# Kernel tuning notes

Hardware: AMD Instinct MI355X
Metric: run time of the kernel (lower is better)

## Reference

```python
import jax, jax.numpy as jnp
import numpy as np

DECAY = 0.25
THRESHOLD = 1.0
TIME_STEPS = 20

@jax.custom_vjp
def spike(v):
    return (v > 0).astype(v.dtype)

def _spike_fwd(v):
    return (v > 0).astype(v.dtype), v

def _spike_bwd(v, g):
    return (g / (1.0 + jnp.abs(v)) ** 2,)

spike.defvjp(_spike_fwd, _spike_bwd)


def setup_inputs() -> dict:
    key = jax.random.key(0)
    k_x, k_w1, k_b1, k_w2, k_b2 = jax.random.split(key, 5)
    B = 32768
    x = jax.random.normal(k_x, (B, 784), dtype=jnp.float32)
    # nn.Linear-style init scales
    W1 = jax.random.normal(k_w1, (128, 784), dtype=jnp.float32) / np.sqrt(784)
    b1 = jax.random.normal(k_b1, (128,), dtype=jnp.float32) / np.sqrt(784)
    W2 = jax.random.normal(k_w2, (10, 128), dtype=jnp.float32) / np.sqrt(128)
    b2 = jax.random.normal(k_b2, (10,), dtype=jnp.float32) / np.sqrt(128)
    return {"x": x, "W1": W1, "b1": b1, "W2": W2, "b2": b2}


def reference(x, W1, b1, W2, b2):
    B = x.shape[0]
    # Input current is constant across timesteps; compute the first GEMM once.
    cur1 = x @ W1.T + b1  # [B, 128]

    def step(carry, _):
        mem1, mem2 = carry
        mem1 = mem1 * DECAY + cur1
        spk1 = spike(mem1 - THRESHOLD)
        mem1 = mem1 * (1.0 - spk1)
        mem2 = mem2 * DECAY + spk1 @ W2.T + b2
        spk2 = spike(mem2 - THRESHOLD)
        mem2 = mem2 * (1.0 - spk2)
        return (mem1, mem2), (spk1, spk2)

    init = (jnp.zeros((B, 128), x.dtype), jnp.zeros((B, 10), x.dtype))
    _, (spk1_rec, spk2_rec) = jax.lax.scan(step, init, None, length=TIME_STEPS)
    output = spk2_rec.sum(axis=0)  # [B, 10]
    return output, spk1_rec  # spk1_rec: [T, B, 128]
```

## Files before the change

### kernel.cpp

```cpp
#include <hip/hip_runtime.h>
#include <cstddef>


constexpr int BROWS  = 64;
constexpr int BK     = 16;
constexpr int NJ     = 128;
constexpr int KDIM   = 784;
constexpr int NO     = 10;
constexpr int TSTEPS = 20;

__global__ __launch_bounds__(256, 2) void snn_fused(
    const float* __restrict__ x,
    const float* __restrict__ W1,
    const float* __restrict__ b1,
    const float* __restrict__ W2,
    const float* __restrict__ b2,
    float* __restrict__ out,
    int B)
{
    __shared__ alignas(16) float xs[BK][68];
    __shared__ alignas(16) float ws[BK][192];
    __shared__ alignas(16) float4 w2s[NJ][3];
    __shared__ unsigned smaskW[2][BROWS][17];
    __shared__ float b2s[12];

    const int t  = threadIdx.x;
    const int tx = t & 15;
    const int ty = t >> 4;
    const int r0 = blockIdx.x * BROWS;

    for (int e = t; e < NJ * 3; e += 256) {
        int og = e % 3, j = e / 3;
        float sc = __int_as_float((127 - (j & 31)) << 23);
        float vv[4];
        #pragma unroll
        for (int c = 0; c < 4; ++c) {
            int o = og * 4 + c;
            vv[c] = (o < NO) ? W2[o * NJ + j] * sc : 0.0f;
        }
        float4 v; v.x = vv[0]; v.y = vv[1]; v.z = vv[2]; v.w = vv[3];
        w2s[j][og] = v;
    }
    if (t < 12) b2s[t] = (t < NO) ? b2[t] : 0.0f;

    float acc[4][8], cur[4][8];
    #pragma unroll
    for (int rr = 0; rr < 4; ++rr)
        #pragma unroll
        for (int jj = 0; jj < 8; ++jj) { acc[rr][jj] = 0.0f; cur[rr][jj] = 0.0f; }

    const int xrow = t >> 2, xkf = (t & 3) * 4;
    const int wj   = t >> 1, wkf = (t & 1) * 8;
    const int wco  = wj >> 3, wci = wj & 7;
    const float* xrp = x  + (size_t)(r0 + xrow) * KDIM + xkf;
    const float* wrp = W1 + (size_t)wj * KDIM + wkf;

    #pragma unroll 1
    for (int tt = 0; tt < 49; ++tt) {
        const int k0 = tt * BK;
        float4 xv = *(const float4*)(xrp + k0);
        float4 wa = *(const float4*)(wrp + k0);
        float4 wb = *(const float4*)(wrp + k0 + 4);
        xs[xkf + 0][xrow] = xv.x; xs[xkf + 1][xrow] = xv.y;
        xs[xkf + 2][xrow] = xv.z; xs[xkf + 3][xrow] = xv.w;
        float* wp0 = &ws[wkf][wco * 12 + wci];
        wp0[0]    = wa.x; wp0[192]  = wa.y; wp0[384]  = wa.z; wp0[576]  = wa.w;
        wp0[768]  = wb.x; wp0[960]  = wb.y; wp0[1152] = wb.z; wp0[1344] = wb.w;
        __syncthreads();
        #pragma unroll
        for (int kk = 0; kk < BK; ++kk) {
            float4 xr  = *(const float4*)&xs[kk][ty * 4];
            float4 wva = *(const float4*)&ws[kk][tx * 12];
            float4 wvb = *(const float4*)&ws[kk][tx * 12 + 4];
            float xf[4] = {xr.x, xr.y, xr.z, xr.w};
            float wf[8] = {wva.x, wva.y, wva.z, wva.w, wvb.x, wvb.y, wvb.z, wvb.w};
            #pragma unroll
            for (int rr = 0; rr < 4; ++rr)
                #pragma unroll
                for (int jj = 0; jj < 8; ++jj)
                    acc[rr][jj] = fmaf(xf[rr], wf[jj], acc[rr][jj]);
        }
        __syncthreads();
        if (tt == 19) {
            #pragma unroll
            for (int rr = 0; rr < 4; ++rr)
                #pragma unroll
                for (int jj = 0; jj < 8; ++jj) { cur[rr][jj] = acc[rr][jj]; acc[rr][jj] = 0.0f; }
        } else if (tt == 39) {
            #pragma unroll
            for (int rr = 0; rr < 4; ++rr)
                #pragma unroll
                for (int jj = 0; jj < 8; ++jj) { cur[rr][jj] = cur[rr][jj] + acc[rr][jj]; acc[rr][jj] = 0.0f; }
        }
    }
    {
        const float* b1p = b1 + tx * 8;
        float4 ba = *(const float4*)b1p, bb = *(const float4*)(b1p + 4);
        float bf[8] = {ba.x, ba.y, ba.z, ba.w, bb.x, bb.y, bb.z, bb.w};
        #pragma unroll
        for (int rr = 0; rr < 4; ++rr)
            #pragma unroll
            for (int jj = 0; jj < 8; ++jj)
                cur[rr][jj] = (cur[rr][jj] + acc[rr][jj]) + bf[jj];
    }

    float mem1[4][8];
    #pragma unroll
    for (int rr = 0; rr < 4; ++rr)
        #pragma unroll
        for (int jj = 0; jj < 8; ++jj) mem1[rr][jj] = 0.0f;

    const int row_l2 = t & 63;
    const int og     = t >> 6;
    float m2[4]  = {0.f, 0.f, 0.f, 0.f};
    float cnt[4] = {0.f, 0.f, 0.f, 0.f};
    float* rec = out + (size_t)B * NO;

    #pragma unroll 1
    for (int st = 0; st < TSTEPS; ++st) {
        const int p = st & 1;
        #pragma unroll
        for (int rr = 0; rr < 4; ++rr) {
            unsigned bt = 0;
            float s0[8];
            #pragma unroll
            for (int jj = 0; jj < 8; ++jj) {
                float m = fmaf(mem1[rr][jj], 0.25f, cur[rr][jj]);
                float v = m - 1.0f;
                bool  s = v > 0.0f;
                s0[jj] = s ? 1.0f : 0.0f;
                mem1[rr][jj] = s ? 0.0f : m;
                bt |= s ? (1u << jj) : 0u;
            }
            size_t base = ((size_t)st * B + (size_t)(r0 + ty * 4 + rr)) * NJ + tx * 8;
            float4 fa; fa.x = s0[0]; fa.y = s0[1]; fa.z = s0[2]; fa.w = s0[3];
            float4 fb; fb.x = s0[4]; fb.y = s0[5]; fb.z = s0[6]; fb.w = s0[7];
            *(float4*)&rec[base]     = fa;
            *(float4*)&rec[base + 4] = fb;
            ((unsigned char*)&smaskW[p][ty * 4 + rr][0])[tx] = (unsigned char)bt;
        }
        __syncthreads();
        if (og < 3) {
            unsigned mw[4];
            #pragma unroll
            for (int w = 0; w < 4; ++w) mw[w] = smaskW[p][row_l2][w];
            float mm[4] = {0.f, 0.f, 0.f, 0.f};
            #pragma unroll
            for (int w = 0; w < 4; ++w) {
                unsigned bits = mw[w];
                #pragma unroll
                for (int b = 0; b < 32; ++b) {
                    float f = (float)(bits & (1u << b));
                    float4 wv = w2s[w * 32 + b][og];
                    mm[0] = fmaf(f, wv.x, mm[0]);
                    mm[1] = fmaf(f, wv.y, mm[1]);
                    mm[2] = fmaf(f, wv.z, mm[2]);
                    mm[3] = fmaf(f, wv.w, mm[3]);
                }
            }
            #pragma unroll
            for (int c = 0; c < 4; ++c) {
                float cur2 = mm[c] + b2s[og * 4 + c];
                float nm   = fmaf(m2[c], 0.25f, cur2);
                float v2   = nm - 1.0f;
                bool  s2   = v2 > 0.0f;
                cnt[c] += s2 ? 1.0f : 0.0f;
                m2[c]  = s2 ? 0.0f : nm;
            }
        }
    }

    if (og < 3) {
        #pragma unroll
        for (int c = 0; c < 4; ++c) {
            int o = og * 4 + c;
            if (o < NO) out[(size_t)(r0 + row_l2) * NO + o] = cnt[c];
        }
    }
}

extern "C" void kernel_launch(void* const* d_in, const int* in_sizes, int n_in,
                              void* d_out, int out_size, void* d_ws, size_t ws_size,
                              hipStream_t stream)
{
    const float* x  = (const float*)d_in[0];
    const float* W1 = (const float*)d_in[1];
    const float* b1 = (const float*)d_in[2];
    const float* W2 = (const float*)d_in[3];
    const float* b2 = (const float*)d_in[4];
    float* out = (float*)d_out;
    const int B = in_sizes[0] / KDIM;
    snn_fused<<<B / BROWS, 256, 0, stream>>>(x, W1, b1, W2, b2, out, B);
}
```

Baseline: 506.9 us.

## Halve row tile, register-prefetch GEMM tiles, use ballot-built spike masks

Shrinks the per-block row tile from 64 to 32, so each thread holds a 4x4 instead of a 4x8 accumulator. Launch bounds rise to 4 blocks per CU for higher occupancy. The next k-tile of x and W1 is prefetched into registers while the current tile is computed. Spike masks for layer 2 are now built with wavefront ballots instead of byte stores into shared memory, and the layer-2 work is split over 64 threads handling 5 outputs each. The cost is a lower arithmetic-to-load ratio in the GEMM (W1 is read twice as often per row) and less parallelism in the layer-2 loop.

```diff
diff --git a/kernel.cpp b/kernel.cpp
--- a/kernel.cpp
+++ b/kernel.cpp
@@ -2,14 +2,14 @@
 #include <cstddef>
 
 
-constexpr int BROWS  = 64;
+constexpr int BROWS  = 32;
 constexpr int BK     = 16;
 constexpr int NJ     = 128;
 constexpr int KDIM   = 784;
 constexpr int NO     = 10;
 constexpr int TSTEPS = 20;
 
-__global__ __launch_bounds__(256, 2) void snn_fused(
+__global__ __launch_bounds__(256, 4) void snn_fused(
     const float* __restrict__ x,
     const float* __restrict__ W1,
     const float* __restrict__ b1,
@@ -18,164 +18,174 @@
     float* __restrict__ out,
     int B)
 {
-    __shared__ alignas(16) float xs[BK][68];
-    __shared__ alignas(16) float ws[BK][192];
-    __shared__ alignas(16) float4 w2s[NJ][3];
-    __shared__ unsigned smaskW[2][BROWS][17];
-    __shared__ float b2s[12];
+    __shared__ alignas(16) float xs[BK][36];
+    __shared__ alignas(16) float ws[BK][140];
+    __shared__ alignas(16) float w2a[NJ][2][8];
+    __shared__ alignas(16) unsigned smask[2][BROWS][4];
 
     const int t  = threadIdx.x;
-    const int tx = t & 15;
-    const int ty = t >> 4;
+    const int tx = t & 31;
+    const int ty = t >> 5;
     const int r0 = blockIdx.x * BROWS;
 
-    for (int e = t; e < NJ * 3; e += 256) {
-        int og = e % 3, j = e / 3;
-        float sc = __int_as_float((127 - (j & 31)) << 23);
-        float vv[4];
-        #pragma unroll
-        for (int c = 0; c < 4; ++c) {
-            int o = og * 4 + c;
-            vv[c] = (o < NO) ? W2[o * NJ + j] * sc : 0.0f;
-        }
-        float4 v; v.x = vv[0]; v.y = vv[1]; v.z = vv[2]; v.w = vv[3];
-        w2s[j][og] = v;
-    }
-    if (t < 12) b2s[t] = (t < NO) ? b2[t] : 0.0f;
-
-    float acc[4][8], cur[4][8];
+    for (int e = t; e < NJ * 16; e += 256) {
+        int c = e & 7, h = (e >> 3) & 1, j = e >> 4;
+        float v = 0.0f;
+        if (c < 5) {
+            float sc = __int_as_float((127 - (j >> 2)) << 23);
+            v = W2[(h * 5 + c) * NJ + j] * sc;
+        }
+        w2a[j][h][c] = v;
+    }
+
+    float acc[4][4], cur[4][4];
     #pragma unroll
     for (int rr = 0; rr < 4; ++rr)
         #pragma unroll
-        for (int jj = 0; jj < 8; ++jj) { acc[rr][jj] = 0.0f; cur[rr][jj] = 0.0f; }
+        for (int cc = 0; cc < 4; ++cc) { acc[rr][cc] = 0.0f; cur[rr][cc] = 0.0f; }
 
     const int xrow = t >> 2, xkf = (t & 3) * 4;
     const int wj   = t >> 1, wkf = (t & 1) * 8;
-    const int wco  = wj >> 3, wci = wj & 7;
+    const int wph  = wj + 4 * (wj >> 5);
     const float* xrp = x  + (size_t)(r0 + xrow) * KDIM + xkf;
     const float* wrp = W1 + (size_t)wj * KDIM + wkf;
 
+    float4 xv, wa, wb;
+    if (t < 128) xv = *(const float4*)(xrp);
+    wa = *(const float4*)(wrp);
+    wb = *(const float4*)(wrp + 4);
+
     #pragma unroll 1
     for (int tt = 0; tt < 49; ++tt) {
-        const int k0 = tt * BK;
-        float4 xv = *(const float4*)(xrp + k0);
-        float4 wa = *(const float4*)(wrp + k0);
-        float4 wb = *(const float4*)(wrp + k0 + 4);
-        xs[xkf + 0][xrow] = xv.x; xs[xkf + 1][xrow] = xv.y;
-        xs[xkf + 2][xrow] = xv.z; xs[xkf + 3][xrow] = xv.w;
-        float* wp0 = &ws[wkf][wco * 12 + wci];
-        wp0[0]    = wa.x; wp0[192]  = wa.y; wp0[384]  = wa.z; wp0[576]  = wa.w;
-        wp0[768]  = wb.x; wp0[960]  = wb.y; wp0[1152] = wb.z; wp0[1344] = wb.w;
+        if (t < 128) {
+            xs[xkf + 0][xrow] = xv.x; xs[xkf + 1][xrow] = xv.y;
+            xs[xkf + 2][xrow] = xv.z; xs[xkf + 3][xrow] = xv.w;
+        }
+        float* wp = &ws[wkf][wph];
+        wp[0]   = wa.x; wp[140] = wa.y; wp[280] = wa.z; wp[420] = wa.w;
+        wp[560] = wb.x; wp[700] = wb.y; wp[840] = wb.z; wp[980] = wb.w;
         __syncthreads();
+        if (tt < 48) {
+            const int k0n = (tt + 1) * BK;
+            if (t < 128) xv = *(const float4*)(xrp + k0n);
+            wa = *(const float4*)(wrp + k0n);
+            wb = *(const float4*)(wrp + k0n + 4);
+        }
         #pragma unroll
         for (int kk = 0; kk < BK; ++kk) {
-            float4 xr  = *(const float4*)&xs[kk][ty * 4];
-            float4 wva = *(const float4*)&ws[kk][tx * 12];
-            float4 wvb = *(const float4*)&ws[kk][tx * 12 + 4];
+            float4 xr = *(const float4*)&xs[kk][ty * 4];
+            float4 wv = *(const float4*)&ws[kk][4 * tx + 4 * (tx >> 3)];
             float xf[4] = {xr.x, xr.y, xr.z, xr.w};
-            float wf[8] = {wva.x, wva.y, wva.z, wva.w, wvb.x, wvb.y, wvb.z, wvb.w};
+            float wf[4] = {wv.x, wv.y, wv.z, wv.w};
             #pragma unroll
             for (int rr = 0; rr < 4; ++rr)
                 #pragma unroll
-                for (int jj = 0; jj < 8; ++jj)
-                    acc[rr][jj] = fmaf(xf[rr], wf[jj], acc[rr][jj]);
+                for (int cc = 0; cc < 4; ++cc)
+                    acc[rr][cc] = fmaf(xf[rr], wf[cc], acc[rr][cc]);
         }
         __syncthreads();
         if (tt == 19) {
             #pragma unroll
             for (int rr = 0; rr < 4; ++rr)
                 #pragma unroll
-                for (int jj = 0; jj < 8; ++jj) { cur[rr][jj] = acc[rr][jj]; acc[rr][jj] = 0.0f; }
+                for (int cc = 0; cc < 4; ++cc) { cur[rr][cc] = acc[rr][cc]; acc[rr][cc] = 0.0f; }
         } else if (tt == 39) {
             #pragma unroll
             for (int rr = 0; rr < 4; ++rr)
                 #pragma unroll
-                for (int jj = 0; jj < 8; ++jj) { cur[rr][jj] = cur[rr][jj] + acc[rr][jj]; acc[rr][jj] = 0.0f; }
+                for (int cc = 0; cc < 4; ++cc) { cur[rr][cc] = cur[rr][cc] + acc[rr][cc]; acc[rr][cc] = 0.0f; }
         }
     }
     {
-        const float* b1p = b1 + tx * 8;
-        float4 ba = *(const float4*)b1p, bb = *(const float4*)(b1p + 4);
-        float bf[8] = {ba.x, ba.y, ba.z, ba.w, bb.x, bb.y, bb.z, bb.w};
+        float4 bv = *(const float4*)(b1 + tx * 4);
+        float bf[4] = {bv.x, bv.y, bv.z, bv.w};
         #pragma unroll
         for (int rr = 0; rr < 4; ++rr)
             #pragma unroll
-            for (int jj = 0; jj < 8; ++jj)
-                cur[rr][jj] = (cur[rr][jj] + acc[rr][jj]) + bf[jj];
-    }
-
-    float mem1[4][8];
+            for (int cc = 0; cc < 4; ++cc)
+                cur[rr][cc] = (cur[rr][cc] + acc[rr][cc]) + bf[cc];
+    }
+
+    float mem1[4][4];
     #pragma unroll
     for (int rr = 0; rr < 4; ++rr)
         #pragma unroll
-        for (int jj = 0; jj < 8; ++jj) mem1[rr][jj] = 0.0f;
-
-    const int row_l2 = t & 63;
-    const int og     = t >> 6;
-    float m2[4]  = {0.f, 0.f, 0.f, 0.f};
-    float cnt[4] = {0.f, 0.f, 0.f, 0.f};
+        for (int cc = 0; cc < 4; ++cc) mem1[rr][cc] = 0.0f;
+
+    const int w  = t >> 6;
+    const int g  = (t >> 5) & 1;
+    const int crow = t & 31;
+    const int ch   = (t >> 5) & 1;
+    float m2[5]  = {0.f, 0.f, 0.f, 0.f, 0.f};
+    float cnt[5] = {0.f, 0.f, 0.f, 0.f, 0.f};
+    float b2r[5];
+    if (t < 64) {
+        #pragma unroll
+        for (int c = 0; c < 5; ++c) b2r[c] = b2[ch * 5 + c];
+    }
     float* rec = out + (size_t)B * NO;
 
     #pragma unroll 1
     for (int st = 0; st < TSTEPS; ++st) {
         const int p = st & 1;
+        bool  sp[4][4];
         #pragma unroll
         for (int rr = 0; rr < 4; ++rr) {
-            unsigned bt = 0;
-            float s0[8];
-            #pragma unroll
-            for (int jj = 0; jj < 8; ++jj) {
-                float m = fmaf(mem1[rr][jj], 0.25f, cur[rr][jj]);
-                float v = m - 1.0f;
-                bool  s = v > 0.0f;
-                s0[jj] = s ? 1.0f : 0.0f;
-                mem1[rr][jj] = s ? 0.0f : m;
-                bt |= s ? (1u << jj) : 0u;
-            }
-            size_t base = ((size_t)st * B + (size_t)(r0 + ty * 4 + rr)) * NJ + tx * 8;
-            float4 fa; fa.x = s0[0]; fa.y = s0[1]; fa.z = s0[2]; fa.w = s0[3];
-            float4 fb; fb.x = s0[4]; fb.y = s0[5]; fb.z = s0[6]; fb.w = s0[7];
-            *(float4*)&rec[base]     = fa;
-            *(float4*)&rec[base + 4] = fb;
-            ((unsigned char*)&smaskW[p][ty * 4 + rr][0])[tx] = (unsigned char)bt;
-        }
+            float s0[4];
+            #pragma unroll
+            for (int cc = 0; cc < 4; ++cc) {
+                float m = fmaf(mem1[rr][cc], 0.25f, cur[rr][cc]);
+                bool  s = (m - 1.0f) > 0.0f;
+                sp[rr][cc] = s;
+                s0[cc] = s ? 1.0f : 0.0f;
+                mem1[rr][cc] = s ? 0.0f : m;
+            }
+            float4 f; f.x = s0[0]; f.y = s0[1]; f.z = s0[2]; f.w = s0[3];
+            *(float4*)&rec[((size_t)st * B + (size_t)(r0 + ty * 4 + rr)) * NJ + tx * 4] = f;
+        }
+        #pragma unroll
+        for (int rr = 0; rr < 4; ++rr)
+            #pragma unroll
+            for (int jj = 0; jj < 4; ++jj) {
+                unsigned long long bm = __ballot(sp[rr][jj]);
+                if ((t & 31) == jj)
+                    smask[p][w * 8 + g * 4 + rr][jj] = (unsigned)(bm >> (g * 32));
+            }
         __syncthreads();
-        if (og < 3) {
-            unsigned mw[4];
-            #pragma unroll
-            for (int w = 0; w < 4; ++w) mw[w] = smaskW[p][row_l2][w];
-            float mm[4] = {0.f, 0.f, 0.f, 0.f};
-            #pragma unroll
-            for (int w = 0; w < 4; ++w) {
-                unsigned bits = mw[w];
-                #pragma unroll
-                for (int b = 0; b < 32; ++b) {
-                    float f = (float)(bits & (1u << b));
-                    float4 wv = w2s[w * 32 + b][og];
-                    mm[0] = fmaf(f, wv.x, mm[0]);
-                    mm[1] = fmaf(f, wv.y, mm[1]);
-                    mm[2] = fmaf(f, wv.z, mm[2]);
-                    mm[3] = fmaf(f, wv.w, mm[3]);
+        if (t < 64) {
+            uint4 mr = *(const uint4*)&smask[p][crow][0];
+            unsigned mw[4] = {mr.x, mr.y, mr.z, mr.w};
+            float mm[5] = {0.f, 0.f, 0.f, 0.f, 0.f};
+            for (int q = 0; q < 32; ++q) {
+                #pragma unroll
+                for (int s = 0; s < 4; ++s) {
+                    int j = 4 * q + s;
+                    float f = (float)(mw[s] & (1u << q));
+                    const float* wp2 = &w2a[j][ch][0];
+                    float4 w4 = *(const float4*)wp2;
+                    float  w5 = wp2[4];
+                    mm[0] = fmaf(f, w4.x, mm[0]);
+                    mm[1] = fmaf(f, w4.y, mm[1]);
+                    mm[2] = fmaf(f, w4.z, mm[2]);
+                    mm[3] = fmaf(f, w4.w, mm[3]);
+                    mm[4] = fmaf(f, w5,   mm[4]);
                 }
             }
             #pragma unroll
-            for (int c = 0; c < 4; ++c) {
-                float cur2 = mm[c] + b2s[og * 4 + c];
+            for (int c = 0; c < 5; ++c) {
+                float cur2 = mm[c] + b2r[c];
                 float nm   = fmaf(m2[c], 0.25f, cur2);
-                float v2   = nm - 1.0f;
-                bool  s2   = v2 > 0.0f;
+                bool  s2   = (nm - 1.0f) > 0.0f;
                 cnt[c] += s2 ? 1.0f : 0.0f;
                 m2[c]  = s2 ? 0.0f : nm;
             }
         }
     }
 
-    if (og < 3) {
-        #pragma unroll
-        for (int c = 0; c < 4; ++c) {
-            int o = og * 4 + c;
-            if (o < NO) out[(size_t)(r0 + row_l2) * NO + o] = cnt[c];
-        }
+    if (t < 64) {
+        #pragma unroll
+        for (int c = 0; c < 5; ++c)
+            out[(size_t)(r0 + crow) * NO + ch * 5 + c] = cnt[c];
     }
 }
 
```

Result: slower. 540.9 us (+6.7%).

## Double-buffer GEMM shared tiles and use nontemporal stores for spike record

Applied to the files above, without the earlier changes.

Splits the shared-memory x and W1 tiles into two buffers and prefetches the next K-tile's global loads into registers while computing on the current tile. This drops one barrier per iteration and hides global load latency behind the FMA loop. The spike record writes also switch to nontemporal stores so the streaming output bypasses cache retention. The second buffer doubles tile LDS use, and the prefetched values raise register pressure under the 2-block launch bound.

```diff
diff --git a/kernel.cpp b/kernel.cpp
--- a/kernel.cpp
+++ b/kernel.cpp
@@ -1,6 +1,8 @@
 #include <hip/hip_runtime.h>
 #include <cstddef>
 
+
+typedef float f32x4 __attribute__((ext_vector_type(4)));
 
 constexpr int BROWS  = 64;
 constexpr int BK     = 16;
@@ -18,8 +20,8 @@
     float* __restrict__ out,
     int B)
 {
-    __shared__ alignas(16) float xs[BK][68];
-    __shared__ alignas(16) float ws[BK][192];
+    __shared__ alignas(16) float xs[2][BK][68];
+    __shared__ alignas(16) float ws[2][BK][192];
     __shared__ alignas(16) float4 w2s[NJ][3];
     __shared__ unsigned smaskW[2][BROWS][17];
     __shared__ float b2s[12];
@@ -55,23 +57,32 @@
     const float* xrp = x  + (size_t)(r0 + xrow) * KDIM + xkf;
     const float* wrp = W1 + (size_t)wj * KDIM + wkf;
 
+    float4 xv = *(const float4*)(xrp);
+    float4 wa = *(const float4*)(wrp);
+    float4 wb = *(const float4*)(wrp + 4);
+    {
+        xs[0][xkf + 0][xrow] = xv.x; xs[0][xkf + 1][xrow] = xv.y;
+        xs[0][xkf + 2][xrow] = xv.z; xs[0][xkf + 3][xrow] = xv.w;
+        float* wp0 = &ws[0][wkf][wco * 12 + wci];
+        wp0[0]    = wa.x; wp0[192]  = wa.y; wp0[384]  = wa.z; wp0[576]  = wa.w;
+        wp0[768]  = wb.x; wp0[960]  = wb.y; wp0[1152] = wb.z; wp0[1344] = wb.w;
+    }
+    __syncthreads();
+
     #pragma unroll 1
     for (int tt = 0; tt < 49; ++tt) {
-        const int k0 = tt * BK;
-        float4 xv = *(const float4*)(xrp + k0);
-        float4 wa = *(const float4*)(wrp + k0);
-        float4 wb = *(const float4*)(wrp + k0 + 4);
-        xs[xkf + 0][xrow] = xv.x; xs[xkf + 1][xrow] = xv.y;
-        xs[xkf + 2][xrow] = xv.z; xs[xkf + 3][xrow] = xv.w;
-        float* wp0 = &ws[wkf][wco * 12 + wci];
-        wp0[0]    = wa.x; wp0[192]  = wa.y; wp0[384]  = wa.z; wp0[576]  = wa.w;
-        wp0[768]  = wb.x; wp0[960]  = wb.y; wp0[1152] = wb.z; wp0[1344] = wb.w;
-        __syncthreads();
+        const int cb = tt & 1;
+        if (tt < 48) {
+            const int k0n = (tt + 1) * BK;
+            xv = *(const float4*)(xrp + k0n);
+            wa = *(const float4*)(wrp + k0n);
+            wb = *(const float4*)(wrp + k0n + 4);
+        }
         #pragma unroll
         for (int kk = 0; kk < BK; ++kk) {
-            float4 xr  = *(const float4*)&xs[kk][ty * 4];
-            float4 wva = *(const float4*)&ws[kk][tx * 12];
-            float4 wvb = *(const float4*)&ws[kk][tx * 12 + 4];
+            float4 xr  = *(const float4*)&xs[cb][kk][ty * 4];
+            float4 wva = *(const float4*)&ws[cb][kk][tx * 12];
+            float4 wvb = *(const float4*)&ws[cb][kk][tx * 12 + 4];
             float xf[4] = {xr.x, xr.y, xr.z, xr.w};
             float wf[8] = {wva.x, wva.y, wva.z, wva.w, wvb.x, wvb.y, wvb.z, wvb.w};
             #pragma unroll
@@ -80,7 +91,6 @@
                 for (int jj = 0; jj < 8; ++jj)
                     acc[rr][jj] = fmaf(xf[rr], wf[jj], acc[rr][jj]);
         }
-        __syncthreads();
         if (tt == 19) {
             #pragma unroll
             for (int rr = 0; rr < 4; ++rr)
@@ -92,6 +102,15 @@
                 #pragma unroll
                 for (int jj = 0; jj < 8; ++jj) { cur[rr][jj] = cur[rr][jj] + acc[rr][jj]; acc[rr][jj] = 0.0f; }
         }
+        if (tt < 48) {
+            const int nb = cb ^ 1;
+            xs[nb][xkf + 0][xrow] = xv.x; xs[nb][xkf + 1][xrow] = xv.y;
+            xs[nb][xkf + 2][xrow] = xv.z; xs[nb][xkf + 3][xrow] = xv.w;
+            float* wp0 = &ws[nb][wkf][wco * 12 + wci];
+            wp0[0]    = wa.x; wp0[192]  = wa.y; wp0[384]  = wa.z; wp0[576]  = wa.w;
+            wp0[768]  = wb.x; wp0[960]  = wb.y; wp0[1152] = wb.z; wp0[1344] = wb.w;
+        }
+        __syncthreads();
     }
     {
         const float* b1p = b1 + tx * 8;
@@ -133,10 +152,10 @@
                 bt |= s ? (1u << jj) : 0u;
             }
             size_t base = ((size_t)st * B + (size_t)(r0 + ty * 4 + rr)) * NJ + tx * 8;
-            float4 fa; fa.x = s0[0]; fa.y = s0[1]; fa.z = s0[2]; fa.w = s0[3];
-            float4 fb; fb.x = s0[4]; fb.y = s0[5]; fb.z = s0[6]; fb.w = s0[7];
-            *(float4*)&rec[base]     = fa;
-            *(float4*)&rec[base + 4] = fb;
+            f32x4 fa = {s0[0], s0[1], s0[2], s0[3]};
+            f32x4 fb = {s0[4], s0[5], s0[6], s0[7]};
+            __builtin_nontemporal_store(fa, (f32x4*)&rec[base]);
+            __builtin_nontemporal_store(fb, (f32x4*)&rec[base + 4]);
             ((unsigned char*)&smaskW[p][ty * 4 + rr][0])[tx] = (unsigned char)bt;
         }
         __syncthreads();
```

New measurement: 498.6 us. About the same (-1.6%).

## Split fused SNN kernel into split-K GEMM and separate spiking dynamics kernel

Applied to the files above, without the earlier changes.

Replaces the single fused kernel with two launches. The first is a split-K GEMM over three K panels, which triples the grid and writes partial sums to workspace. The second is a spiking kernel that uses 16-row blocks, sums the partials with the bias, and runs the 20 timesteps with one row per thread group and one output per thread for the second layer. The aim is more parallelism and occupancy than the fused kernel, which had only 512 blocks and did a serial 784-deep reduction. The cost is a 3×B×128 float round trip through workspace and an extra launch. The old fused kernel remains as a fallback when the workspace is too small.

```diff
diff --git a/kernel.cpp b/kernel.cpp
--- a/kernel.cpp
+++ b/kernel.cpp
@@ -8,8 +8,175 @@
 constexpr int KDIM   = 784;
 constexpr int NO     = 10;
 constexpr int TSTEPS = 20;
-
-__global__ __launch_bounds__(256, 2) void snn_fused(
+constexpr int BR2    = 16;
+
+__global__ __launch_bounds__(256, 4) void gemm_panel(
+    const float* __restrict__ x,
+    const float* __restrict__ W1,
+    float* __restrict__ pout,
+    int B)
+{
+    __shared__ alignas(16) float xs[BK][68];
+    __shared__ alignas(16) float ws[BK][192];
+
+    const int t  = threadIdx.x;
+    const int tx = t & 15;
+    const int ty = t >> 4;
+    const int r0 = blockIdx.x * BROWS;
+    const int p  = blockIdx.y;
+    const int kbase = p * 320;
+    const int NT = (p < 2) ? 20 : 9;
+
+    float acc[4][8];
+    #pragma unroll
+    for (int rr = 0; rr < 4; ++rr)
+        #pragma unroll
+        for (int jj = 0; jj < 8; ++jj) acc[rr][jj] = 0.0f;
+
+    const int xrow = t >> 2, xkf = (t & 3) * 4;
+    const int wj   = t >> 1, wkf = (t & 1) * 8;
+    const int wco  = wj >> 3, wci = wj & 7;
+    const float* xrp = x  + (size_t)(r0 + xrow) * KDIM + kbase + xkf;
+    const float* wrp = W1 + (size_t)wj * KDIM + kbase + wkf;
+
+    #pragma unroll 1
+    for (int tt = 0; tt < NT; ++tt) {
+        const int k0 = tt * BK;
+        float4 xv = *(const float4*)(xrp + k0);
+        float4 wa = *(const float4*)(wrp + k0);
+        float4 wb = *(const float4*)(wrp + k0 + 4);
+        xs[xkf + 0][xrow] = xv.x; xs[xkf + 1][xrow] = xv.y;
+        xs[xkf + 2][xrow] = xv.z; xs[xkf + 3][xrow] = xv.w;
+        float* wp0 = &ws[wkf][wco * 12 + wci];
+        wp0[0]    = wa.x; wp0[192]  = wa.y; wp0[384]  = wa.z; wp0[576]  = wa.w;
+        wp0[768]  = wb.x; wp0[960]  = wb.y; wp0[1152] = wb.z; wp0[1344] = wb.w;
+        __syncthreads();
+        #pragma unroll
+        for (int kk = 0; kk < BK; ++kk) {
+            float4 xr  = *(const float4*)&xs[kk][ty * 4];
+            float4 wva = *(const float4*)&ws[kk][tx * 12];
+            float4 wvb = *(const float4*)&ws[kk][tx * 12 + 4];
+            float xf[4] = {xr.x, xr.y, xr.z, xr.w};
+            float wf[8] = {wva.x, wva.y, wva.z, wva.w, wvb.x, wvb.y, wvb.z, wvb.w};
+            #pragma unroll
+            for (int rr = 0; rr < 4; ++rr)
+                #pragma unroll
+                for (int jj = 0; jj < 8; ++jj)
+                    acc[rr][jj] = fmaf(xf[rr], wf[jj], acc[rr][jj]);
+        }
+        __syncthreads();
+    }
+
+    float* dst = pout + (size_t)p * B * NJ;
+    #pragma unroll
+    for (int rr = 0; rr < 4; ++rr) {
+        size_t base = (size_t)(r0 + ty * 4 + rr) * NJ + tx * 8;
+        float4 fa; fa.x = acc[rr][0]; fa.y = acc[rr][1]; fa.z = acc[rr][2]; fa.w = acc[rr][3];
+        float4 fb; fb.x = acc[rr][4]; fb.y = acc[rr][5]; fb.z = acc[rr][6]; fb.w = acc[rr][7];
+        *(float4*)&dst[base]     = fa;
+        *(float4*)&dst[base + 4] = fb;
+    }
+}
+
+__global__ __launch_bounds__(256, 4) void snn_dyn(
+    const float* __restrict__ pout,
+    const float* __restrict__ b1,
+    const float* __restrict__ W2,
+    const float* __restrict__ b2,
+    float* __restrict__ out,
+    int B)
+{
+    __shared__ float w2v[NJ][12];
+    __shared__ unsigned smask[2][BR2][20];
+
+    const int t  = threadIdx.x;
+    const int tx = t & 15;
+    const int ty = t >> 4;
+    const int r0 = blockIdx.x * BR2;
+
+    for (int e = t; e < NJ * NO; e += 256) {
+        int o = e >> 7, j = e & 127;
+        float sc = __int_as_float((127 - (j & 31)) << 23);
+        w2v[j][o] = W2[o * NJ + j] * sc;
+    }
+
+    const size_t ps = (size_t)B * NJ;
+    const float* prow = pout + (size_t)(r0 + ty) * NJ + tx * 8;
+    float4 p1a = *(const float4*)(prow);
+    float4 p1b = *(const float4*)(prow + 4);
+    float4 p2a = *(const float4*)(prow + ps);
+    float4 p2b = *(const float4*)(prow + ps + 4);
+    float4 p3a = *(const float4*)(prow + 2 * ps);
+    float4 p3b = *(const float4*)(prow + 2 * ps + 4);
+    float4 ba  = *(const float4*)(b1 + tx * 8);
+    float4 bb  = *(const float4*)(b1 + tx * 8 + 4);
+    float cur[8], mem1[8];
+    {
+        float p1[8] = {p1a.x, p1a.y, p1a.z, p1a.w, p1b.x, p1b.y, p1b.z, p1b.w};
+        float p2[8] = {p2a.x, p2a.y, p2a.z, p2a.w, p2b.x, p2b.y, p2b.z, p2b.w};
+        float p3[8] = {p3a.x, p3a.y, p3a.z, p3a.w, p3b.x, p3b.y, p3b.z, p3b.w};
+        float bf[8] = {ba.x, ba.y, ba.z, ba.w, bb.x, bb.y, bb.z, bb.w};
+        #pragma unroll
+        for (int jj = 0; jj < 8; ++jj) {
+            cur[jj]  = ((p1[jj] + p2[jj]) + p3[jj]) + bf[jj];
+            mem1[jj] = 0.0f;
+        }
+    }
+
+    const bool cons = (t < 160);
+    const int  crow = t / 10;
+    const int  co   = t - crow * 10;
+    float m2 = 0.0f, cnt = 0.0f;
+    float b2o = cons ? b2[co] : 0.0f;
+    float* rec = out + (size_t)B * NO;
+
+    __syncthreads();
+
+    #pragma unroll 1
+    for (int st = 0; st < TSTEPS; ++st) {
+        const int p = st & 1;
+        unsigned bt = 0;
+        float s0[8];
+        #pragma unroll
+        for (int jj = 0; jj < 8; ++jj) {
+            float m = fmaf(mem1[jj], 0.25f, cur[jj]);
+            bool  s = (m - 1.0f) > 0.0f;
+            s0[jj] = s ? 1.0f : 0.0f;
+            mem1[jj] = s ? 0.0f : m;
+            bt |= s ? (1u << jj) : 0u;
+        }
+        size_t base = ((size_t)st * B + (size_t)(r0 + ty)) * NJ + tx * 8;
+        float4 fa; fa.x = s0[0]; fa.y = s0[1]; fa.z = s0[2]; fa.w = s0[3];
+        float4 fb; fb.x = s0[4]; fb.y = s0[5]; fb.z = s0[6]; fb.w = s0[7];
+        *(float4*)&rec[base]     = fa;
+        *(float4*)&rec[base + 4] = fb;
+        ((unsigned char*)&smask[p][ty][0])[tx] = (unsigned char)bt;
+        __syncthreads();
+        if (cons) {
+            uint4 mr = *(const uint4*)&smask[p][crow][0];
+            unsigned mw[4] = {mr.x, mr.y, mr.z, mr.w};
+            float mm = 0.0f;
+            #pragma unroll
+            for (int w = 0; w < 4; ++w) {
+                unsigned bits = mw[w];
+                #pragma unroll
+                for (int b = 0; b < 32; ++b) {
+                    float f = (float)(bits & (1u << b));
+                    mm = fmaf(f, w2v[w * 32 + b][co], mm);
+                }
+            }
+            float cur2 = mm + b2o;
+            float nm   = fmaf(m2, 0.25f, cur2);
+            bool  s2   = (nm - 1.0f) > 0.0f;
+            cnt += s2 ? 1.0f : 0.0f;
+            m2  = s2 ? 0.0f : nm;
+        }
+    }
+
+    if (cons) out[(size_t)(r0 + crow) * NO + co] = cnt;
+}
+
+__global__ __launch_bounds__(256, 2) void snn_fused_fb(
     const float* __restrict__ x,
     const float* __restrict__ W1,
     const float* __restrict__ b1,
@@ -190,5 +357,13 @@
     const float* b2 = (const float*)d_in[4];
     float* out = (float*)d_out;
     const int B = in_sizes[0] / KDIM;
-    snn_fused<<<B / BROWS, 256, 0, stream>>>(x, W1, b1, W2, b2, out, B);
+
+    const size_t need = (size_t)3 * B * NJ * sizeof(float);
+    if (ws_size >= need) {
+        dim3 g1(B / BROWS, 3);
+        gemm_panel<<<g1, 256, 0, stream>>>(x, W1, (float*)d_ws, B);
+        snn_dyn<<<B / BR2, 256, 0, stream>>>((const float*)d_ws, b1, W2, b2, out, B);
+    } else {
+        snn_fused_fb<<<B / BROWS, 256, 0, stream>>>(x, W1, b1, W2, b2, out, B);
+    }
 }
```

Result: no change. 506.3 us (-0.1%).
